# Performance work log

Hardware: AMD Instinct MI355X
Metric: run time of the kernel (lower is better)

The kernel has to match this reference:

```python
import jax, jax.numpy as jnp
import numpy as np

N, IN, H, C, E = 50000, 128, 2, 64, 800000
HC = H * C  # 128
NEG_SLOPE = 0.2
EPS_GN = 1e-5


def setup_inputs() -> dict:
    key = jax.random.key(0)
    ks = jax.random.split(key, 32)
    r = lambda i, shape: jax.random.normal(ks[i], shape, dtype=jnp.float32) * 0.1
    inp = {
        'x': jax.random.normal(ks[0], (N, IN), dtype=jnp.float32),
        'edge_index': jax.random.randint(ks[1], (2, E), 0, N, dtype=jnp.int64),
        # conv 0: in=128 -> heads*emb=128
        'Wl0': r(2, (IN, HC)), 'bl0': jnp.zeros((HC,), jnp.float32),
        'Wr0': r(3, (IN, HC)), 'br0': jnp.zeros((HC,), jnp.float32),
        'att0': r(4, (H, C)), 'bias0': jnp.zeros((HC,), jnp.float32),
        # conv 1: in=128 -> 128
        'Wl1': r(5, (HC, HC)), 'bl1': jnp.zeros((HC,), jnp.float32),
        'Wr1': r(6, (HC, HC)), 'br1': jnp.zeros((HC,), jnp.float32),
        'att1': r(7, (H, C)), 'bias1': jnp.zeros((HC,), jnp.float32),
        # GraphNorm params (weight, bias, mean_scale)
        'g0': jnp.ones((HC,), jnp.float32), 'be0': jnp.zeros((HC,), jnp.float32), 'ms0': jnp.ones((HC,), jnp.float32),
        'g1': jnp.ones((HC,), jnp.float32), 'be1': jnp.zeros((HC,), jnp.float32), 'ms1': jnp.ones((HC,), jnp.float32),
        # MLP head
        'W1': r(8, (HC, C)), 'b1': jnp.zeros((C,), jnp.float32),
        'W2': r(9, (C, 2)), 'b2': jnp.zeros((2,), jnp.float32),
    }
    return inp


def gatv2_conv(x, src, dst, Wl, bl, Wr, br, att, bias):
    # PyG GATv2Conv: separate source/target transforms, edge attention, segment softmax
    xl = (x @ Wl + bl).reshape(N, H, C)  # source features
    xr = (x @ Wr + br).reshape(N, H, C)  # target features
    m = jax.nn.leaky_relu(xl[src] + xr[dst], NEG_SLOPE)  # [Etot, H, C]
    e = jnp.einsum('ehc,hc->eh', m, att)                  # [Etot, H]
    emax = jax.ops.segment_max(e, dst, num_segments=N)    # stable softmax per dst
    ex = jnp.exp(e - emax[dst])
    denom = jax.ops.segment_sum(ex, dst, num_segments=N)
    alpha = ex / (denom[dst] + 1e-16)
    out = jax.ops.segment_sum(xl[src] * alpha[:, :, None], dst, num_segments=N)
    return out.reshape(N, HC) + bias


def graph_norm(x, gamma, beta, mean_scale):
    # PyG GraphNorm with batch=None (single graph)
    mean = x.mean(axis=0)
    out = x - mean_scale * mean
    var = (out * out).mean(axis=0)
    return gamma * out / jnp.sqrt(var + EPS_GN) + beta


def reference(x, edge_index, Wl0, bl0, Wr0, br0, att0, bias0,
              Wl1, bl1, Wr1, br1, att1, bias1,
              g0, be0, ms0, g1, be1, ms1, W1, b1, W2, b2):
    loop = jnp.arange(N, dtype=edge_index.dtype)
    src = jnp.concatenate([edge_index[0], loop])  # add_self_loops=True
    dst = jnp.concatenate([edge_index[1], loop])
    # layer 0 (conv + GraphNorm + ReLU)
    h = jax.nn.relu(graph_norm(gatv2_conv(x, src, dst, Wl0, bl0, Wr0, br0, att0, bias0), g0, be0, ms0))
    # layer 1
    h = jax.nn.relu(graph_norm(gatv2_conv(h, src, dst, Wl1, bl1, Wr1, br1, att1, bias1), g1, be1, ms1))
    # dropout is identity in eval mode
    h = jax.nn.relu(h @ W1 + b1)
    return h @ W2 + b2
```

## Files before the change

### kernel.cpp

```cpp
#include <hip/hip_runtime.h>
#include <hip/hip_bf16.h>

#define N_NODES 50000
#define NE      800000
#define NETOT   (NE + N_NODES)
#define NEG     0.2f
#define NBUCK   196
#define NSEG    64
#define SEGCAP  128
#define NCTR    (NBUCK * NSEG)

typedef unsigned short u16;
typedef unsigned int   u32;
typedef __attribute__((ext_vector_type(8))) short bf16x8;
typedef __attribute__((ext_vector_type(4))) float f32x4;

__device__ __forceinline__ float b2f(u16 v) {
    union { float f; u32 u; } c; c.u = ((u32)v) << 16; return c.f;
}
__device__ __forceinline__ u16 f2b(float f) {
    union { float f; u32 u; } c; c.f = f;
    u32 r = c.u + 0x7FFF + ((c.u >> 16) & 1);
    return (u16)(r >> 16);
}
__device__ __forceinline__ float ldf(const void* p, int i, int fmt) {
    return fmt ? b2f(((const u16*)p)[i]) : ((const float*)p)[i];
}

__global__ void init_all(const u32* __restrict__ xw, const u32* __restrict__ w0,
                         const int* __restrict__ ei,
                         int* __restrict__ flag, int* __restrict__ bcnt) {
    int g = blockIdx.x * 256 + threadIdx.x;
    if (g < NCTR) bcnt[g] = 0;
    if (blockIdx.x == 0) {
        int wv = threadIdx.x >> 6, l = threadIdx.x & 63;
        if (wv == 0) {
            u32 v = xw[l * 50000 + 1];
            u32 e = (v >> 7) & 0xFF;
            unsigned long long m = __ballot(e >= 100 && e <= 140);
            if (l == 0) { flag[0] = (__popcll(m) >= 48) ? 1 : 0; flag[1] = 0; }
        } else if (wv == 1) {
            u32 v = w0[l * 128 + 1];
            u32 e = (v >> 7) & 0xFF;
            unsigned long long m = __ballot(e >= 100 && e <= 140);
            if (l == 0) flag[3] = (__popcll(m) >= 48) ? 1 : 0;
        } else if (wv == 2) {
            int v = ei[(l * 25000) | 1];
            unsigned long long nz = __ballot(v != 0);
            if (l == 0) flag[2] = (nz == 0ULL) ? 1 : 0;
        }
    }
}

__global__ void bin_a(const int* __restrict__ ei, const int* __restrict__ flag,
                      int* __restrict__ bcnt, u32* __restrict__ pairs) {
    int e = blockIdx.x * 256 + threadIdx.x;
    if (e >= NE) return;
    int f = flag[2];
    int s, d;
    if (f) { s = ei[2 * e]; d = ei[2 * (NE + e)]; }
    else   { s = ei[e];     d = ei[NE + e]; }
    int idx = (d >> 8) * NSEG + (blockIdx.x & (NSEG - 1));
    int pos = atomicAdd(&bcnt[idx], 1);
    if (pos < SEGCAP)
        pairs[(size_t)idx * SEGCAP + pos] = ((u32)(d & 255) << 16) | (u32)s;
}

__global__ void bucket_scan(const int* __restrict__ bcnt, int* __restrict__ bbase,
                            int* __restrict__ indptr) {
    __shared__ int sh[256];
    int tid = threadIdx.x;
    int tot = 0;
    if (tid < NBUCK) {
        int nb0 = tid << 8;
        int nodes = min(256, N_NODES - nb0);
        int edges = 0;
        for (int seg = 0; seg < NSEG; ++seg)
            edges += min(bcnt[tid * NSEG + seg], SEGCAP);
        tot = edges + nodes;
    }
    sh[tid] = tot; __syncthreads();
    for (int off = 1; off < 256; off <<= 1) {
        int u = (tid >= off) ? sh[tid - off] : 0;
        __syncthreads();
        sh[tid] += u;
        __syncthreads();
    }
    if (tid < NBUCK) bbase[tid] = sh[tid] - tot;
    if (tid == 0) indptr[N_NODES] = sh[NBUCK - 1];
}

__global__ __launch_bounds__(256) void bin_b(const u32* __restrict__ pairs,
        const int* __restrict__ bcnt, const int* __restrict__ bbase,
        int* __restrict__ indptr, int* __restrict__ srcs) {
    __shared__ int cnt[256];
    __shared__ int scn[256];
    __shared__ int msh[NSEG];
    int b = blockIdx.x, tid = threadIdx.x;
    int nb0 = b << 8;
    int nodesHere = min(256, N_NODES - nb0);
    if (tid < NSEG) msh[tid] = min(bcnt[b * NSEG + tid], SEGCAP);
    cnt[tid] = (tid < nodesHere) ? 1 : 0;
    __syncthreads();
    const u32* bp = pairs + (size_t)b * NSEG * SEGCAP;
    for (int t = tid; t < NSEG * SEGCAP; t += 256) {
        int seg = t >> 7, i = t & (SEGCAP - 1);
        if (i < msh[seg]) {
            int dloc = (int)(bp[t] >> 16);
            atomicAdd(&cnt[dloc], 1);
        }
    }
    __syncthreads();
    int v = cnt[tid];
    scn[tid] = v; __syncthreads();
    for (int off = 1; off < 256; off <<= 1) {
        int u = (tid >= off) ? scn[tid - off] : 0;
        __syncthreads();
        scn[tid] += u;
        __syncthreads();
    }
    int myoff = bbase[b] + scn[tid] - v;
    if (tid < nodesHere) indptr[nb0 + tid] = myoff;
    __syncthreads();
    cnt[tid] = myoff;
    __syncthreads();
    if (tid < nodesHere) {
        int pos = atomicAdd(&cnt[tid], 1);
        srcs[pos] = nb0 + tid;
    }
    for (int t = tid; t < NSEG * SEGCAP; t += 256) {
        int seg = t >> 7, i = t & (SEGCAP - 1);
        if (i < msh[seg]) {
            u32 p = bp[t];
            int pos = atomicAdd(&cnt[p >> 16], 1);
            srcs[pos] = (int)(p & 0xffff);
        }
    }
}

#define LDP 136
__global__ __launch_bounds__(256) void gemm_xf(const void* __restrict__ inp,
        const int* __restrict__ fin, const int* __restrict__ fw,
        const void* __restrict__ Wl, const void* __restrict__ bl,
        const void* __restrict__ Wr, const void* __restrict__ br,
        const float* __restrict__ nscale, const float* __restrict__ nshift,
        u16* __restrict__ XL, u16* __restrict__ XR) {
    __shared__ u16 As16[64 * LDP];
    __shared__ u16 Bs16[128 * LDP];
    __shared__ float Sc[128], Sh[128];
    int fi = fin[0], fb = fw[0];
    int by = blockIdx.y;
    const void* W  = by ? Wr : Wl;
    const void* bi = by ? br : bl;
    u16* dst       = by ? XR : XL;
    int n0 = blockIdx.x * 64;
    int tid = threadIdx.x;
    bool donorm = (nscale != nullptr);
    if (donorm) {
        if (tid < 128) { Sc[tid] = nscale[tid]; Sh[tid] = nshift[tid]; }
        __syncthreads();
    }
    if (fi) {
        for (int t = tid; t < 64 * 16; t += 256) {
            int node = t >> 4, c8 = (t & 15) << 3;
            int n = n0 + node;
            bf16x8 v = {0,0,0,0,0,0,0,0};
            if (n < N_NODES) v = *(const bf16x8*)((const u16*)inp + (size_t)n * 128 + c8);
            *(bf16x8*)&As16[node * LDP + c8] = v;
        }
    } else {
        for (int t = tid; t < 64 * 32; t += 256) {
            int node = t >> 5, c4 = (t & 31) << 2;
            int n = n0 + node;
            float4 v = {0.f, 0.f, 0.f, 0.f};
            if (n < N_NODES) v = *(const float4*)((const float*)inp + (size_t)n * 128 + c4);
            if (donorm) {
                v.x = fmaxf(v.x * Sc[c4]     + Sh[c4],     0.f);
                v.y = fmaxf(v.y * Sc[c4 + 1] + Sh[c4 + 1], 0.f);
                v.z = fmaxf(v.z * Sc[c4 + 2] + Sh[c4 + 2], 0.f);
                v.w = fmaxf(v.w * Sc[c4 + 3] + Sh[c4 + 3], 0.f);
            }
            ushort4 h;
            h.x = f2b(v.x); h.y = f2b(v.y); h.z = f2b(v.z); h.w = f2b(v.w);
            *(ushort4*)&As16[node * LDP + c4] = h;
        }
    }
    if (fb) {
        for (int t = tid; t < 128 * 16; t += 256) {
            int k = t >> 4, j8 = (t & 15) << 3;
            bf16x8 v = *(const bf16x8*)((const u16*)W + k * 128 + j8);
            #pragma unroll
            for (int q = 0; q < 8; ++q) Bs16[(j8 + q) * LDP + k] = (u16)v[q];
        }
    } else {
        for (int t = tid; t < 128 * 32; t += 256) {
            int k = t >> 5, j4 = (t & 31) << 2;
            float4 v = *(const float4*)((const float*)W + k * 128 + j4);
            Bs16[(j4 + 0) * LDP + k] = f2b(v.x);
            Bs16[(j4 + 1) * LDP + k] = f2b(v.y);
            Bs16[(j4 + 2) * LDP + k] = f2b(v.z);
            Bs16[(j4 + 3) * LDP + k] = f2b(v.w);
        }
    }
    __syncthreads();

    int wv = tid >> 6, lane = tid & 63;
    int quad = lane >> 4, r = lane & 15;
    int m0 = wv * 16;
    f32x4 acc[8] = {{0.f,0.f,0.f,0.f},{0.f,0.f,0.f,0.f},{0.f,0.f,0.f,0.f},
                    {0.f,0.f,0.f,0.f},{0.f,0.f,0.f,0.f},{0.f,0.f,0.f,0.f},
                    {0.f,0.f,0.f,0.f},{0.f,0.f,0.f,0.f}};
    #pragma unroll
    for (int ks = 0; ks < 4; ++ks) {
        int ko = ks * 32 + quad * 8;
        bf16x8 af = *(const bf16x8*)&As16[(m0 + r) * LDP + ko];
        #pragma unroll
        for (int jt = 0; jt < 8; ++jt) {
            bf16x8 bfr = *(const bf16x8*)&Bs16[(jt * 16 + r) * LDP + ko];
            acc[jt] = __builtin_amdgcn_mfma_f32_16x16x32_bf16(af, bfr, acc[jt], 0, 0, 0);
        }
    }
    __syncthreads();
    #pragma unroll
    for (int jt = 0; jt < 8; ++jt) {
        int j = jt * 16 + r;
        float bj = ldf(bi, j, fb);
        #pragma unroll
        for (int reg = 0; reg < 4; ++reg) {
            As16[(m0 + quad * 4 + reg) * LDP + j] = f2b(acc[jt][reg] + bj);
        }
    }
    __syncthreads();
    #pragma unroll
    for (int rep = 0; rep < 4; ++rep) {
        int idx = rep * 256 + tid;
        int node = idx >> 4, c8 = (idx & 15) << 3;
        int n = n0 + node;
        if (n < N_NODES) {
            bf16x8 v = *(const bf16x8*)&As16[node * LDP + c8];
            *(bf16x8*)(dst + (size_t)n * 128 + c8) = v;
        }
    }
}

__global__ __launch_bounds__(64) void agg_kernel(const u16* __restrict__ XL,
        const u16* __restrict__ XR, const void* __restrict__ att,
        const int* __restrict__ fmt,
        const int* __restrict__ indptr, const int* __restrict__ srcs,
        float4* __restrict__ OUT4) {
    int lane = threadIdx.x;
    int n = blockIdx.x;
    int eh = lane >> 5, q = lane & 31;
    int fb = fmt[0];
    ushort4 xrv = *(const ushort4*)(XR + (size_t)n * 128 + q * 4);
    float xr0 = b2f(xrv.x), xr1 = b2f(xrv.y), xr2 = b2f(xrv.z), xr3 = b2f(xrv.w);
    float a0 = ldf(att, 4 * q,     fb);
    float a1 = ldf(att, 4 * q + 1, fb);
    float a2 = ldf(att, 4 * q + 2, fb);
    float a3 = ldf(att, 4 * q + 3, fb);
    int beg = indptr[n], end = indptr[n + 1];
    float acc0 = 0.f, acc1 = 0.f, acc2 = 0.f, acc3 = 0.f, dsum = 0.f;
    int nit = (end - beg + 5) / 6;
    for (int it = 0; it < nit; ++it) {
        int iA = beg + 6 * it + eh;
        int iB = iA + 2;
        int iC = iA + 4;
        bool vA = (iA < end), vB = (iB < end), vC = (iC < end);
        int sA = vA ? srcs[iA] : 0;
        int sB = vB ? srcs[iB] : 0;
        int sC = vC ? srcs[iC] : 0;
        ushort4 xa = *(const ushort4*)(XL + (size_t)sA * 128 + q * 4);
        ushort4 xb = *(const ushort4*)(XL + (size_t)sB * 128 + q * 4);
        ushort4 xc = *(const ushort4*)(XL + (size_t)sC * 128 + q * 4);
        float A0 = b2f(xa.x), A1 = b2f(xa.y), A2 = b2f(xa.z), A3 = b2f(xa.w);
        float B0 = b2f(xb.x), B1 = b2f(xb.y), B2v = b2f(xb.z), B3 = b2f(xb.w);
        float C0 = b2f(xc.x), C1 = b2f(xc.y), C2 = b2f(xc.z), C3 = b2f(xc.w);
        float tA0 = A0 + xr0; tA0 = fmaxf(tA0, 0.f) + NEG * fminf(tA0, 0.f);
        float tA1 = A1 + xr1; tA1 = fmaxf(tA1, 0.f) + NEG * fminf(tA1, 0.f);
        float tA2 = A2 + xr2; tA2 = fmaxf(tA2, 0.f) + NEG * fminf(tA2, 0.f);
        float tA3 = A3 + xr3; tA3 = fmaxf(tA3, 0.f) + NEG * fminf(tA3, 0.f);
        float tB0 = B0 + xr0; tB0 = fmaxf(tB0, 0.f) + NEG * fminf(tB0, 0.f);
        float tB1 = B1 + xr1; tB1 = fmaxf(tB1, 0.f) + NEG * fminf(tB1, 0.f);
        float tB2 = B2v + xr2; tB2 = fmaxf(tB2, 0.f) + NEG * fminf(tB2, 0.f);
        float tB3 = B3 + xr3; tB3 = fmaxf(tB3, 0.f) + NEG * fminf(tB3, 0.f);
        float tC0 = C0 + xr0; tC0 = fmaxf(tC0, 0.f) + NEG * fminf(tC0, 0.f);
        float tC1 = C1 + xr1; tC1 = fmaxf(tC1, 0.f) + NEG * fminf(tC1, 0.f);
        float tC2 = C2 + xr2; tC2 = fmaxf(tC2, 0.f) + NEG * fminf(tC2, 0.f);
        float tC3 = C3 + xr3; tC3 = fmaxf(tC3, 0.f) + NEG * fminf(tC3, 0.f);
        float pA = tA0 * a0;
        pA = fmaf(tA1, a1, pA); pA = fmaf(tA2, a2, pA); pA = fmaf(tA3, a3, pA);
        float pB = tB0 * a0;
        pB = fmaf(tB1, a1, pB); pB = fmaf(tB2, a2, pB); pB = fmaf(tB3, a3, pB);
        float pC = tC0 * a0;
        pC = fmaf(tC1, a1, pC); pC = fmaf(tC2, a2, pC); pC = fmaf(tC3, a3, pC);
        pA += __shfl_xor(pA, 1);  pB += __shfl_xor(pB, 1);  pC += __shfl_xor(pC, 1);
        pA += __shfl_xor(pA, 2);  pB += __shfl_xor(pB, 2);  pC += __shfl_xor(pC, 2);
        pA += __shfl_xor(pA, 4);  pB += __shfl_xor(pB, 4);  pC += __shfl_xor(pC, 4);
        pA += __shfl_xor(pA, 8);  pB += __shfl_xor(pB, 8);  pC += __shfl_xor(pC, 8);
        float wA = vA ? __expf(fminf(pA, 60.f)) : 0.f;
        float wB = vB ? __expf(fminf(pB, 60.f)) : 0.f;
        float wC = vC ? __expf(fminf(pC, 60.f)) : 0.f;
        acc0 = fmaf(wA, A0, acc0); acc1 = fmaf(wA, A1, acc1);
        acc2 = fmaf(wA, A2, acc2); acc3 = fmaf(wA, A3, acc3);
        acc0 = fmaf(wB, B0, acc0); acc1 = fmaf(wB, B1, acc1);
        acc2 = fmaf(wB, B2v, acc2); acc3 = fmaf(wB, B3, acc3);
        acc0 = fmaf(wC, C0, acc0); acc1 = fmaf(wC, C1, acc1);
        acc2 = fmaf(wC, C2, acc2); acc3 = fmaf(wC, C3, acc3);
        dsum += wA + wB + wC;
    }
    acc0 += __shfl_xor(acc0, 32);
    acc1 += __shfl_xor(acc1, 32);
    acc2 += __shfl_xor(acc2, 32);
    acc3 += __shfl_xor(acc3, 32);
    dsum += __shfl_xor(dsum, 32);
    if (eh == 0) {
        float inv = 1.f / (dsum + 1e-16f);
        float4 o; o.x = acc0 * inv; o.y = acc1 * inv; o.z = acc2 * inv; o.w = acc3 * inv;
        OUT4[(size_t)n * 32 + q] = o;
    }
}

__global__ __launch_bounds__(256) void colstats(const float* __restrict__ OUT,
        const void* __restrict__ bias, const int* __restrict__ fmt,
        float* __restrict__ Sp1, float* __restrict__ Sp2) {
    __shared__ float sh1[256], sh2[256];
    int tid = threadIdx.x;
    int c = tid & 127, half = tid >> 7;
    float bf = ldf(bias, c, fmt[0]);
    float s1 = 0.f, s2 = 0.f;
    for (int r = blockIdx.x * 2 + half; r < N_NODES; r += gridDim.x * 2) {
        float t = OUT[r * 128 + c] + bf;
        s1 += t; s2 += t * t;
    }
    sh1[tid] = s1; sh2[tid] = s2; __syncthreads();
    if (tid < 128) {
        Sp1[blockIdx.x * 128 + tid] = sh1[tid] + sh1[tid + 128];
        Sp2[blockIdx.x * 128 + tid] = sh2[tid] + sh2[tid + 128];
    }
}

__global__ __launch_bounds__(256) void finalize_norm(const float* __restrict__ Sp1,
        const float* __restrict__ Sp2,
        const void* __restrict__ gamma, const void* __restrict__ beta,
        const void* __restrict__ msc, const void* __restrict__ bias,
        const int* __restrict__ fmt,
        float* __restrict__ scaleA, float* __restrict__ shiftB) {
    __shared__ float sh1[256], sh2[256];
    int c = blockIdx.x, tid = threadIdx.x;
    sh1[tid] = Sp1[tid * 128 + c];
    sh2[tid] = Sp2[tid * 128 + c];
    __syncthreads();
    for (int off = 128; off > 0; off >>= 1) {
        if (tid < off) { sh1[tid] += sh1[tid + off]; sh2[tid] += sh2[tid + off]; }
        __syncthreads();
    }
    if (tid == 0) {
        int fb = fmt[0];
        const float invN = 1.f / (float)N_NODES;
        float mean = sh1[0] * invN;
        float ex2  = sh2[0] * invN;
        float ms = ldf(msc, c, fb);
        float var = ex2 - 2.f * ms * mean * mean + ms * ms * mean * mean;
        float rstd = rsqrtf(var + 1e-5f);
        float A = ldf(gamma, c, fb) * rstd;
        scaleA[c] = A;
        shiftB[c] = ldf(beta, c, fb) - A * (ms * mean - ldf(bias, c, fb));
    }
}

__global__ __launch_bounds__(256) void mlp_kernel(const float* __restrict__ H,
        const void* __restrict__ w1, const void* __restrict__ b1,
        const void* __restrict__ w2, const void* __restrict__ b2,
        const float* __restrict__ nscale, const float* __restrict__ nshift,
        const int* __restrict__ fmt,
        float* __restrict__ out) {
    __shared__ float W1s[128 * 64];
    __shared__ float W2s[128];
    __shared__ float b1s[64];
    __shared__ float Sc[128], Sh[128];
    int tid = threadIdx.x;
    int fb = fmt[0];
    if (fb) {
        for (int t = tid; t < 128 * 8; t += 256) {
            int row8 = t << 3;
            bf16x8 v = *(const bf16x8*)((const u16*)w1 + row8);
            #pragma unroll
            for (int q = 0; q < 8; ++q) W1s[row8 + q] = b2f((u16)v[q]);
        }
    } else {
        for (int t = tid; t < 128 * 64; t += 256) W1s[t] = ((const float*)w1)[t];
    }
    if (tid < 128) { W2s[tid] = ldf(w2, tid, fb); Sc[tid] = nscale[tid]; Sh[tid] = nshift[tid]; }
    if (tid < 64)  b1s[tid] = ldf(b1, tid, fb);
    __syncthreads();
    int n = blockIdx.x * 256 + tid;
    if (n >= N_NODES) return;
    float z[64];
    #pragma unroll
    for (int j = 0; j < 64; j++) z[j] = b1s[j];
    for (int kb = 0; kb < 128; kb += 16) {
        float h[16];
        #pragma unroll
        for (int t = 0; t < 4; t++) {
            float4 v = *(const float4*)&H[n * 128 + kb + t * 4];
            int c = kb + t * 4;
            h[4 * t]     = fmaxf(v.x * Sc[c]     + Sh[c],     0.f);
            h[4 * t + 1] = fmaxf(v.y * Sc[c + 1] + Sh[c + 1], 0.f);
            h[4 * t + 2] = fmaxf(v.z * Sc[c + 2] + Sh[c + 2], 0.f);
            h[4 * t + 3] = fmaxf(v.w * Sc[c + 3] + Sh[c + 3], 0.f);
        }
        #pragma unroll
        for (int i = 0; i < 16; i++) {
            float hv = h[i];
            const float* wrow = &W1s[(kb + i) * 64];
            #pragma unroll
            for (int j = 0; j < 64; j += 4) {
                const float4 w = *(const float4*)&wrow[j];
                z[j]     += hv * w.x;
                z[j + 1] += hv * w.y;
                z[j + 2] += hv * w.z;
                z[j + 3] += hv * w.w;
            }
        }
    }
    float o0 = ldf(b2, 0, fb), o1 = ldf(b2, 1, fb);
    #pragma unroll
    for (int j = 0; j < 64; j++) {
        float zr = fmaxf(z[j], 0.f);
        o0 += zr * W2s[j * 2];
        o1 += zr * W2s[j * 2 + 1];
    }
    if (o0 != o0) o0 = 12345.f;
    if (o1 != o1) o1 = 12345.f;
    float2 o; o.x = o0; o.y = o1;
    ((float2*)out)[n] = o;
}

extern "C" void kernel_launch(void* const* d_in, const int* in_sizes, int n_in,
                              void* d_out, int out_size, void* d_ws, size_t ws_size,
                              hipStream_t stream) {
    (void)in_sizes; (void)n_in; (void)out_size; (void)ws_size;
    const void* x    = d_in[0];
    const int*  ei   = (const int*)d_in[1];
    const void* Wl0  = d_in[2];
    const void* bl0  = d_in[3];
    const void* Wr0  = d_in[4];
    const void* br0  = d_in[5];
    const void* att0 = d_in[6];
    const void* bias0= d_in[7];
    const void* Wl1  = d_in[8];
    const void* bl1  = d_in[9];
    const void* Wr1  = d_in[10];
    const void* br1  = d_in[11];
    const void* att1 = d_in[12];
    const void* bias1= d_in[13];
    const void* g0   = d_in[14];
    const void* be0  = d_in[15];
    const void* ms0  = d_in[16];
    const void* g1   = d_in[17];
    const void* be1  = d_in[18];
    const void* ms1  = d_in[19];
    const void* W1   = d_in[20];
    const void* b1   = d_in[21];
    const void* W2   = d_in[22];
    const void* b2   = d_in[23];

    char* ws = (char*)d_ws;
    const size_t NF2 = (size_t)N_NODES * 128 * 2;
    const size_t NF4 = (size_t)N_NODES * 128 * 4;
    u16*   XLb = (u16*)(ws);
    u16*   XRb = (u16*)(ws + NF2);
    float* B2  = (float*)(ws + 2 * NF2);
    u32*   pairs = (u32*)B2;
    char* small = ws + 2 * NF2 + NF4;
    float* scaleA = (float*)(small + 1024);
    float* shiftB = (float*)(small + 1536);
    int*   flag   = (int*)(small + 2048);
    int*   bbase  = (int*)(small + 2112);
    float* Sp1    = (float*)(small + 4096);
    float* Sp2    = (float*)(small + 4096 + 131072);
    int*   bcnt   = (int*)(small + 4096 + 262144);
    int*   indptr = (int*)(small + 4096 + 262144 + 50176);
    int*   srcs   = indptr + (N_NODES + 64);

    const int* fX   = &flag[0];
    const int* fFP  = &flag[1];
    const int* fPar = &flag[3];

    init_all<<<(NCTR + 255) / 256, 256, 0, stream>>>((const u32*)x, (const u32*)Wl0,
                                                     ei, flag, bcnt);
    bin_a<<<(NE + 255) / 256, 256, 0, stream>>>(ei, flag, bcnt, pairs);
    bucket_scan<<<1, 256, 0, stream>>>(bcnt, bbase, indptr);
    bin_b<<<NBUCK, 256, 0, stream>>>(pairs, bcnt, bbase, indptr, srcs);

    dim3 ggemm((N_NODES + 63) / 64, 2);

    for (int layer = 0; layer < 2; ++layer) {
        const void* Wl = layer ? Wl1 : Wl0;  const void* bl = layer ? bl1 : bl0;
        const void* Wr = layer ? Wr1 : Wr0;  const void* br = layer ? br1 : br0;
        const void* at = layer ? att1 : att0;
        const void* bi = layer ? bias1 : bias0;
        const void* gm = layer ? g1 : g0;    const void* bt = layer ? be1 : be0;
        const void* mS = layer ? ms1 : ms0;
        const void* inp = layer ? (const void*)B2 : x;
        const int* fin  = layer ? fFP : fX;
        const float* ns = layer ? scaleA : nullptr;
        const float* nh = layer ? shiftB : nullptr;

        gemm_xf<<<ggemm, 256, 0, stream>>>(inp, fin, fPar, Wl, bl, Wr, br, ns, nh,
                                           XLb, XRb);
        agg_kernel<<<N_NODES, 64, 0, stream>>>(XLb, XRb, at, fPar, indptr, srcs,
                                               (float4*)B2);
        colstats<<<256, 256, 0, stream>>>(B2, bi, fPar, Sp1, Sp2);
        finalize_norm<<<128, 256, 0, stream>>>(Sp1, Sp2, gm, bt, mS, bi, fPar,
                                               scaleA, shiftB);
    }

    mlp_kernel<<<(N_NODES + 255) / 256, 256, 0, stream>>>(B2, W1, b1, W2, b2,
                                                          scaleA, shiftB, fPar,
                                                          (float*)d_out);
}
```

Baseline: 452.6 us.

## Fold bucket scan into bin_b, fuse colstats with finalize, enlarge GEMM tile

Removes the single-block bucket_scan launch: each bin_b block now computes its own base offset by summing the bucket counts before it. colstats and finalize_norm become one kernel in which the last block to finish, detected with an atomic counter, reduces the partials and writes the norm scale and shift. The grid grows to 512 blocks with larger partial buffers. The node GEMM tile is doubled to 128 rows so each wave computes two 16-row MFMA tiles and reuses every B fragment twice. Together this cuts launches and per-launch overhead at the cost of redundant prefix-sum reads in bin_b, more shared memory per GEMM block, and fewer GEMM blocks.

```diff
diff --git a/kernel.cpp b/kernel.cpp
--- a/kernel.cpp
+++ b/kernel.cpp
@@ -9,6 +9,7 @@
 #define NSEG    64
 #define SEGCAP  128
 #define NCTR    (NBUCK * NSEG)
+#define CSG     512
 
 typedef unsigned short u16;
 typedef unsigned int   u32;
@@ -38,7 +39,10 @@
             u32 v = xw[l * 50000 + 1];
             u32 e = (v >> 7) & 0xFF;
             unsigned long long m = __ballot(e >= 100 && e <= 140);
-            if (l == 0) { flag[0] = (__popcll(m) >= 48) ? 1 : 0; flag[1] = 0; }
+            if (l == 0) {
+                flag[0] = (__popcll(m) >= 48) ? 1 : 0;
+                flag[1] = 0; flag[8] = 0; flag[9] = 0;
+            }
         } else if (wv == 1) {
             u32 v = w0[l * 128 + 1];
             u32 e = (v >> 7) & 0xFF;
@@ -66,40 +70,27 @@
         pairs[(size_t)idx * SEGCAP + pos] = ((u32)(d & 255) << 16) | (u32)s;
 }
 
-__global__ void bucket_scan(const int* __restrict__ bcnt, int* __restrict__ bbase,
-                            int* __restrict__ indptr) {
-    __shared__ int sh[256];
-    int tid = threadIdx.x;
-    int tot = 0;
-    if (tid < NBUCK) {
-        int nb0 = tid << 8;
-        int nodes = min(256, N_NODES - nb0);
-        int edges = 0;
-        for (int seg = 0; seg < NSEG; ++seg)
-            edges += min(bcnt[tid * NSEG + seg], SEGCAP);
-        tot = edges + nodes;
-    }
-    sh[tid] = tot; __syncthreads();
-    for (int off = 1; off < 256; off <<= 1) {
-        int u = (tid >= off) ? sh[tid - off] : 0;
-        __syncthreads();
-        sh[tid] += u;
-        __syncthreads();
-    }
-    if (tid < NBUCK) bbase[tid] = sh[tid] - tot;
-    if (tid == 0) indptr[N_NODES] = sh[NBUCK - 1];
-}
-
 __global__ __launch_bounds__(256) void bin_b(const u32* __restrict__ pairs,
-        const int* __restrict__ bcnt, const int* __restrict__ bbase,
+        const int* __restrict__ bcnt,
         int* __restrict__ indptr, int* __restrict__ srcs) {
     __shared__ int cnt[256];
     __shared__ int scn[256];
     __shared__ int msh[NSEG];
+    __shared__ int baseSh;
     int b = blockIdx.x, tid = threadIdx.x;
     int nb0 = b << 8;
     int nodesHere = min(256, N_NODES - nb0);
     if (tid < NSEG) msh[tid] = min(bcnt[b * NSEG + tid], SEGCAP);
+    int pre = 0;
+    for (int i = tid; i < b * NSEG; i += 256) pre += min(bcnt[i], SEGCAP);
+    scn[tid] = pre; __syncthreads();
+    for (int off = 128; off > 0; off >>= 1) {
+        if (tid < off) scn[tid] += scn[tid + off];
+        __syncthreads();
+    }
+    if (tid == 0) baseSh = scn[0] + nb0;
+    __syncthreads();
+    int base = baseSh;
     cnt[tid] = (tid < nodesHere) ? 1 : 0;
     __syncthreads();
     const u32* bp = pairs + (size_t)b * NSEG * SEGCAP;
@@ -119,8 +110,9 @@
         scn[tid] += u;
         __syncthreads();
     }
-    int myoff = bbase[b] + scn[tid] - v;
+    int myoff = base + scn[tid] - v;
     if (tid < nodesHere) indptr[nb0 + tid] = myoff;
+    if (tid == 255 && b == NBUCK - 1) indptr[N_NODES] = base + scn[255];
     __syncthreads();
     cnt[tid] = myoff;
     __syncthreads();
@@ -139,13 +131,14 @@
 }
 
 #define LDP 136
+#define NT  128
 __global__ __launch_bounds__(256) void gemm_xf(const void* __restrict__ inp,
         const int* __restrict__ fin, const int* __restrict__ fw,
         const void* __restrict__ Wl, const void* __restrict__ bl,
         const void* __restrict__ Wr, const void* __restrict__ br,
         const float* __restrict__ nscale, const float* __restrict__ nshift,
         u16* __restrict__ XL, u16* __restrict__ XR) {
-    __shared__ u16 As16[64 * LDP];
+    __shared__ u16 As16[NT * LDP];
     __shared__ u16 Bs16[128 * LDP];
     __shared__ float Sc[128], Sh[128];
     int fi = fin[0], fb = fw[0];
@@ -153,7 +146,7 @@
     const void* W  = by ? Wr : Wl;
     const void* bi = by ? br : bl;
     u16* dst       = by ? XR : XL;
-    int n0 = blockIdx.x * 64;
+    int n0 = blockIdx.x * NT;
     int tid = threadIdx.x;
     bool donorm = (nscale != nullptr);
     if (donorm) {
@@ -161,7 +154,7 @@
         __syncthreads();
     }
     if (fi) {
-        for (int t = tid; t < 64 * 16; t += 256) {
+        for (int t = tid; t < NT * 16; t += 256) {
             int node = t >> 4, c8 = (t & 15) << 3;
             int n = n0 + node;
             bf16x8 v = {0,0,0,0,0,0,0,0};
@@ -169,7 +162,7 @@
             *(bf16x8*)&As16[node * LDP + c8] = v;
         }
     } else {
-        for (int t = tid; t < 64 * 32; t += 256) {
+        for (int t = tid; t < NT * 32; t += 256) {
             int node = t >> 5, c4 = (t & 31) << 2;
             int n = n0 + node;
             float4 v = {0.f, 0.f, 0.f, 0.f};
@@ -206,18 +199,22 @@
 
     int wv = tid >> 6, lane = tid & 63;
     int quad = lane >> 4, r = lane & 15;
-    int m0 = wv * 16;
-    f32x4 acc[8] = {{0.f,0.f,0.f,0.f},{0.f,0.f,0.f,0.f},{0.f,0.f,0.f,0.f},
-                    {0.f,0.f,0.f,0.f},{0.f,0.f,0.f,0.f},{0.f,0.f,0.f,0.f},
-                    {0.f,0.f,0.f,0.f},{0.f,0.f,0.f,0.f}};
+    int m0 = wv * 32;
+    f32x4 acc[2][8];
+    #pragma unroll
+    for (int mt = 0; mt < 2; ++mt)
+        #pragma unroll
+        for (int jt = 0; jt < 8; ++jt) acc[mt][jt] = (f32x4){0.f, 0.f, 0.f, 0.f};
     #pragma unroll
     for (int ks = 0; ks < 4; ++ks) {
         int ko = ks * 32 + quad * 8;
-        bf16x8 af = *(const bf16x8*)&As16[(m0 + r) * LDP + ko];
+        bf16x8 af0 = *(const bf16x8*)&As16[(m0 + r) * LDP + ko];
+        bf16x8 af1 = *(const bf16x8*)&As16[(m0 + 16 + r) * LDP + ko];
         #pragma unroll
         for (int jt = 0; jt < 8; ++jt) {
             bf16x8 bfr = *(const bf16x8*)&Bs16[(jt * 16 + r) * LDP + ko];
-            acc[jt] = __builtin_amdgcn_mfma_f32_16x16x32_bf16(af, bfr, acc[jt], 0, 0, 0);
+            acc[0][jt] = __builtin_amdgcn_mfma_f32_16x16x32_bf16(af0, bfr, acc[0][jt], 0, 0, 0);
+            acc[1][jt] = __builtin_amdgcn_mfma_f32_16x16x32_bf16(af1, bfr, acc[1][jt], 0, 0, 0);
         }
     }
     __syncthreads();
@@ -226,13 +223,16 @@
         int j = jt * 16 + r;
         float bj = ldf(bi, j, fb);
         #pragma unroll
-        for (int reg = 0; reg < 4; ++reg) {
-            As16[(m0 + quad * 4 + reg) * LDP + j] = f2b(acc[jt][reg] + bj);
+        for (int mt = 0; mt < 2; ++mt) {
+            #pragma unroll
+            for (int reg = 0; reg < 4; ++reg) {
+                As16[(m0 + mt * 16 + quad * 4 + reg) * LDP + j] = f2b(acc[mt][jt][reg] + bj);
+            }
         }
     }
     __syncthreads();
     #pragma unroll
-    for (int rep = 0; rep < 4; ++rep) {
+    for (int rep = 0; rep < 8; ++rep) {
         int idx = rep * 256 + tid;
         int node = idx >> 4, c8 = (idx & 15) << 3;
         int n = n0 + node;
@@ -320,13 +320,18 @@
     }
 }
 
-__global__ __launch_bounds__(256) void colstats(const float* __restrict__ OUT,
-        const void* __restrict__ bias, const int* __restrict__ fmt,
-        float* __restrict__ Sp1, float* __restrict__ Sp2) {
+__global__ __launch_bounds__(256) void colstats_fin(const float* __restrict__ OUT,
+        const void* __restrict__ bias,
+        const void* __restrict__ gamma, const void* __restrict__ beta,
+        const void* __restrict__ msc, const int* __restrict__ fmt,
+        float* __restrict__ Sp1, float* __restrict__ Sp2, int* __restrict__ ctr,
+        float* __restrict__ scaleA, float* __restrict__ shiftB) {
     __shared__ float sh1[256], sh2[256];
+    __shared__ int lastsh;
     int tid = threadIdx.x;
     int c = tid & 127, half = tid >> 7;
-    float bf = ldf(bias, c, fmt[0]);
+    int fb = fmt[0];
+    float bf = ldf(bias, c, fb);
     float s1 = 0.f, s2 = 0.f;
     for (int r = blockIdx.x * 2 + half; r < N_NODES; r += gridDim.x * 2) {
         float t = OUT[r * 128 + c] + bf;
@@ -337,34 +342,33 @@
         Sp1[blockIdx.x * 128 + tid] = sh1[tid] + sh1[tid + 128];
         Sp2[blockIdx.x * 128 + tid] = sh2[tid] + sh2[tid + 128];
     }
-}
-
-__global__ __launch_bounds__(256) void finalize_norm(const float* __restrict__ Sp1,
-        const float* __restrict__ Sp2,
-        const void* __restrict__ gamma, const void* __restrict__ beta,
-        const void* __restrict__ msc, const void* __restrict__ bias,
-        const int* __restrict__ fmt,
-        float* __restrict__ scaleA, float* __restrict__ shiftB) {
-    __shared__ float sh1[256], sh2[256];
-    int c = blockIdx.x, tid = threadIdx.x;
-    sh1[tid] = Sp1[tid * 128 + c];
-    sh2[tid] = Sp2[tid * 128 + c];
-    __syncthreads();
-    for (int off = 128; off > 0; off >>= 1) {
-        if (tid < off) { sh1[tid] += sh1[tid + off]; sh2[tid] += sh2[tid + off]; }
-        __syncthreads();
-    }
+    __threadfence();
+    __syncthreads();
     if (tid == 0) {
-        int fb = fmt[0];
+        int old = atomicAdd(ctr, 1);
+        lastsh = (old == (int)gridDim.x - 1) ? 1 : 0;
+    }
+    __syncthreads();
+    if (!lastsh) return;
+    __threadfence();
+    float t1 = 0.f, t2 = 0.f;
+    for (int b = half; b < (int)gridDim.x; b += 2) {
+        t1 += Sp1[b * 128 + c];
+        t2 += Sp2[b * 128 + c];
+    }
+    sh1[tid] = t1; sh2[tid] = t2; __syncthreads();
+    if (tid < 128) {
+        float S1 = sh1[tid] + sh1[tid + 128];
+        float S2 = sh2[tid] + sh2[tid + 128];
         const float invN = 1.f / (float)N_NODES;
-        float mean = sh1[0] * invN;
-        float ex2  = sh2[0] * invN;
-        float ms = ldf(msc, c, fb);
+        float mean = S1 * invN;
+        float ex2  = S2 * invN;
+        float ms = ldf(msc, tid, fb);
         float var = ex2 - 2.f * ms * mean * mean + ms * ms * mean * mean;
         float rstd = rsqrtf(var + 1e-5f);
-        float A = ldf(gamma, c, fb) * rstd;
-        scaleA[c] = A;
-        shiftB[c] = ldf(beta, c, fb) - A * (ms * mean - ldf(bias, c, fb));
+        float A = ldf(gamma, tid, fb) * rstd;
+        scaleA[tid] = A;
+        shiftB[tid] = ldf(beta, tid, fb) - A * (ms * mean - bf);
     }
 }
 
@@ -476,11 +480,10 @@
     float* scaleA = (float*)(small + 1024);
     float* shiftB = (float*)(small + 1536);
     int*   flag   = (int*)(small + 2048);
-    int*   bbase  = (int*)(small + 2112);
     float* Sp1    = (float*)(small + 4096);
-    float* Sp2    = (float*)(small + 4096 + 131072);
-    int*   bcnt   = (int*)(small + 4096 + 262144);
-    int*   indptr = (int*)(small + 4096 + 262144 + 50176);
+    float* Sp2    = (float*)(small + 4096 + 262144);
+    int*   bcnt   = (int*)(small + 4096 + 524288);
+    int*   indptr = (int*)(small + 4096 + 524288 + 50176);
     int*   srcs   = indptr + (N_NODES + 64);
 
     const int* fX   = &flag[0];
@@ -490,10 +493,9 @@
     init_all<<<(NCTR + 255) / 256, 256, 0, stream>>>((const u32*)x, (const u32*)Wl0,
                                                      ei, flag, bcnt);
     bin_a<<<(NE + 255) / 256, 256, 0, stream>>>(ei, flag, bcnt, pairs);
-    bucket_scan<<<1, 256, 0, stream>>>(bcnt, bbase, indptr);
-    bin_b<<<NBUCK, 256, 0, stream>>>(pairs, bcnt, bbase, indptr, srcs);
-
-    dim3 ggemm((N_NODES + 63) / 64, 2);
+    bin_b<<<NBUCK, 256, 0, stream>>>(pairs, bcnt, indptr, srcs);
+
+    dim3 ggemm((N_NODES + NT - 1) / NT, 2);
 
     for (int layer = 0; layer < 2; ++layer) {
         const void* Wl = layer ? Wl1 : Wl0;  const void* bl = layer ? bl1 : bl0;
@@ -511,9 +513,9 @@
                                            XLb, XRb);
         agg_kernel<<<N_NODES, 64, 0, stream>>>(XLb, XRb, at, fPar, indptr, srcs,
                                                (float4*)B2);
-        colstats<<<256, 256, 0, stream>>>(B2, bi, fPar, Sp1, Sp2);
-        finalize_norm<<<128, 256, 0, stream>>>(Sp1, Sp2, gm, bt, mS, bi, fPar,
-                                               scaleA, shiftB);
+        colstats_fin<<<CSG, 256, 0, stream>>>(B2, bi, gm, bt, mS, fPar,
+                                              Sp1, Sp2, &flag[8 + layer],
+                                              scaleA, shiftB);
     }
 
     mlp_kernel<<<(N_NODES + 255) / 256, 256, 0, stream>>>(B2, W1, b1, W2, b2,
```

Result: slower. 615.2 us (+35.9%).
